# Optimization experiments

Hardware: AMD Instinct MI355X
Metric: run time of the kernel (lower is better)

## Reference

```python
import jax, jax.numpy as jnp
import numpy as np

RES = (512, 512)
MAX_VAL = 100.0
OBJ_WIDTH = 5
N_ITERS = 5
SIGMA = 0.2


def setup_inputs() -> dict:
    key = jax.random.key(0)
    ks = jax.random.split(key, 6)
    H, W = RES
    x = jax.random.uniform(ks[0], (1, H, W, 2), jnp.float32) * 2.0 - 1.0  # query grid in [-1,1]
    boundary_types = jax.random.randint(ks[1], (H, W), 0, 2, jnp.int32)
    boundary_conditions = jax.random.uniform(ks[2], (H, W), jnp.float32)
    B_enc = SIGMA * jax.random.normal(ks[3], (64, 2), jnp.float32)  # GaussianEncoding(0.2, 2, 64)
    Wh = jax.random.normal(ks[4], (4, 128, 128), jnp.float32) / jnp.sqrt(128.0)
    W_out = jax.random.normal(ks[5], (128, 1), jnp.float32) / jnp.sqrt(128.0)
    return {"x": x, "boundary_types": boundary_types,
            "boundary_conditions": boundary_conditions,
            "B_enc": B_enc, "Wh": Wh, "W_out": W_out}


def _box_filter(a, width):
    # width x width mean filter, 'same' padding (F.conv2d with ones/width^2 kernel)
    k = jnp.ones((1, 1, width, width), a.dtype) / float(width * width)
    return jax.lax.conv_general_dilated(a[None, None], k, (1, 1), "SAME")[0, 0]


def _grid_sample_2d(img, grid):
    # img [H,W]; grid [N,2] with (x,y) in [-1,1]; bilinear, align_corners=True, border padding
    H, W = img.shape
    ix = jnp.clip((grid[:, 0] + 1.0) * 0.5 * (W - 1), 0.0, W - 1.0)
    iy = jnp.clip((grid[:, 1] + 1.0) * 0.5 * (H - 1), 0.0, H - 1.0)
    x0 = jnp.floor(ix).astype(jnp.int32)
    y0 = jnp.floor(iy).astype(jnp.int32)
    x1 = jnp.clip(x0 + 1, 0, W - 1)
    y1 = jnp.clip(y0 + 1, 0, H - 1)
    wx = ix - x0
    wy = iy - y0
    return (img[y0, x0] * (1 - wx) * (1 - wy) + img[y0, x1] * wx * (1 - wy)
            + img[y1, x0] * (1 - wx) * wy + img[y1, x1] * wx * wy)


def _solve(V0, C, boundary_types, boundary_conditions):
    # 5 Jacobi-style 8-neighbor stencil passes: free cells take the neighbor
    # average plus local cost; boundary cells are pinned to their conditions.
    free = boundary_types == 0

    def step(V, _):
        Vp = jnp.pad(V, 1, mode="edge")
        nb = (Vp[:-2, :-2] + Vp[:-2, 1:-1] + Vp[:-2, 2:]
              + Vp[1:-1, :-2] + Vp[1:-1, 2:]
              + Vp[2:, :-2] + Vp[2:, 1:-1] + Vp[2:, 2:]) / 8.0
        return jnp.where(free, nb + C, boundary_conditions), None

    V, _ = jax.lax.scan(step, V0, None, length=N_ITERS)
    return V


def reference(x, boundary_types, boundary_conditions, B_enc, Wh, W_out):
    H, W = RES
    free = boundary_types == 0
    # V init: max_val everywhere, boundary cells pinned (obj_inds = boundary_types > 0)
    V0 = jnp.where(free, jnp.float32(MAX_VAL), boundary_conditions)

    # Gaussian random Fourier feature encoding of 0.5 + 0.5*x -> 128 dims
    xq = 0.5 + 0.5 * x.reshape(-1, 2)
    vp = (2.0 * jnp.pi) * (xq @ B_enc.T)            # [N, 64]
    enc = jnp.concatenate([jnp.cos(vp), jnp.sin(vp)], axis=-1)  # [N, 128]

    # FullyFusedMLP: 4 hidden ReLU layers of 128 neurons, linear 1-dim output, no bias
    h = enc
    for i in range(Wh.shape[0]):
        h = jax.nn.relu(h @ Wh[i])
    C = (h @ W_out).reshape(H, W)
    C_pos = jax.nn.relu(C)

    # extra cost: box-filtered obstacle boundary values splashed onto free cells
    obj = boundary_conditions * (boundary_types == 1) * (boundary_conditions > 0)
    extra = _box_filter(obj, OBJ_WIDTH) * free
    Cs = C_pos + extra

    out_grid = _solve(V0, Cs, boundary_types, boundary_conditions)
    out = _grid_sample_2d(out_grid, x.reshape(-1, 2)).reshape(H, W)
    return out, C
```

## Files before the change

### kernel.cpp

```cpp
#include <hip/hip_runtime.h>
#include <hip/hip_bf16.h>


typedef unsigned short ushort_t;
typedef short short8 __attribute__((ext_vector_type(8)));
typedef float floatx4 __attribute__((ext_vector_type(4)));

#define HH 512
#define WW 512
#define NPIX (HH*WW)

#define SW(p, f) (((p) << 7) + (((((f) >> 3) ^ ((p) & 15))) << 3) + ((f) & 7))

__device__ inline unsigned int pk_bf16(float a, float b) {
    __hip_bfloat162 h = __float22bfloat162_rn(float2{a, b});
    return *(unsigned int*)&h;
}
__device__ inline float bf2f(ushort_t u) {
    union { unsigned int i; float f; } v; v.i = ((unsigned int)u) << 16; return v.f;
}
__device__ inline void async_copy16(void* lds, const void* g) {
    __builtin_amdgcn_global_load_lds(
        (const __attribute__((address_space(1))) unsigned int*)g,
        (__attribute__((address_space(3))) unsigned int*)lds, 16, 0, 0);
}

__global__ __launch_bounds__(256) void prep_kernel(const float* __restrict__ Wh,
                                                   ushort_t* __restrict__ WT) {
    __shared__ float trans[64 * 33];
    const int tid = threadIdx.x;
    const int l = blockIdx.x >> 3, ng = (blockIdx.x >> 2) & 1, kq = blockIdx.x & 3;
    const int n0 = ng * 64, k0 = kq * 32;
    const int ln = tid & 63, wv = tid >> 6;
    #pragma unroll
    for (int pass = 0; pass < 8; ++pass) {
        int k = k0 + pass * 4 + wv;
        trans[ln * 33 + (k - k0)] = Wh[l * 16384 + k * 128 + n0 + ln];
    }
    __syncthreads();
    {
        int nl = tid >> 2, q = tid & 3;
        int n = n0 + nl;
        int lc = kq * 4 + q;
        int pc = lc ^ (n & 15);
        unsigned int w[4];
        #pragma unroll
        for (int j = 0; j < 4; ++j)
            w[j] = pk_bf16(trans[nl * 33 + q * 8 + 2 * j], trans[nl * 33 + q * 8 + 2 * j + 1]);
        *(uint4*)&WT[(l * 128 + n) * 128 + pc * 8] = uint4{w[0], w[1], w[2], w[3]};
    }
}

__global__ __launch_bounds__(256, 2) void mlp_kernel(const float* __restrict__ x,
                                                     const ushort_t* __restrict__ WT,
                                                     const float* __restrict__ benc,
                                                     const float* __restrict__ wout,
                                                     float* __restrict__ C_ws,
                                                     float* __restrict__ outbuf) {
    __shared__ __align__(16) ushort_t act[128 * 128];
    __shared__ __align__(16) ushort_t wbuf[128 * 128];
    const int tid = threadIdx.x;
    const int p0 = blockIdx.x * 128;
    const int lane = tid & 63, wave = tid >> 6;

    {
        const char* src = (const char*)WT;
        int base = wave * 512;
        #pragma unroll
        for (int c2 = 0; c2 < 8; ++c2) {
            int cb = base + c2 * 64;
            async_copy16(&wbuf[cb * 8], src + (cb + lane) * 16);
        }
    }

    {
        int p = tid & 127, h = tid >> 7;
        float2 xv = ((const float2*)x)[p0 + p];
        float xq0 = 0.5f + 0.5f * xv.x, xq1 = 0.5f + 0.5f * xv.y;
        const float4* b4 = (const float4*)benc;
        #pragma unroll 4
        for (int f2 = 0; f2 < 32; f2 += 2) {
            int f = h * 32 + f2;
            float4 b = b4[f >> 1];
            float t0 = __builtin_amdgcn_fractf(xq0 * b.x + xq1 * b.y);
            float t1 = __builtin_amdgcn_fractf(xq0 * b.z + xq1 * b.w);
            float s0 = __builtin_amdgcn_sinf(t0), c0 = __builtin_amdgcn_cosf(t0);
            float s1 = __builtin_amdgcn_sinf(t1), c1 = __builtin_amdgcn_cosf(t1);
            *(unsigned int*)&act[SW(p, f)]      = pk_bf16(c0, c1);
            *(unsigned int*)&act[SW(p, f + 64)] = pk_bf16(s0, s1);
        }
    }

    const int quad = lane >> 4, l16 = lane & 15;
    const int ntb = (wave >> 1) * 64;
    const int ptb = (wave & 1) * 64;

    #pragma unroll 1
    for (int l = 0; l < 4; ++l) {
        __syncthreads();

        floatx4 acc[4][4];
        #pragma unroll
        for (int i = 0; i < 4; ++i)
            #pragma unroll
            for (int j = 0; j < 4; ++j)
                acc[i][j] = floatx4{0.0f, 0.0f, 0.0f, 0.0f};

        #pragma unroll
        for (int ks = 0; ks < 4; ++ks) {
            int cs = ks * 4 + quad;
            short8 af[4], bv[4];
            #pragma unroll
            for (int i = 0; i < 4; ++i) {
                int r = ntb + i * 16 + l16;
                af[i] = *(const short8*)&wbuf[(r << 7) + ((cs ^ l16) << 3)];
            }
            #pragma unroll
            for (int j = 0; j < 4; ++j) {
                int p = ptb + j * 16 + l16;
                bv[j] = *(const short8*)&act[(p << 7) + ((cs ^ l16) << 3)];
            }
            #pragma unroll
            for (int i = 0; i < 4; ++i)
                #pragma unroll
                for (int j = 0; j < 4; ++j)
                    acc[i][j] = __builtin_amdgcn_mfma_f32_16x16x32_bf16(af[i], bv[j], acc[i][j], 0, 0, 0);
        }
        __syncthreads();

        if (l < 3) {
            const char* src = (const char*)WT + (l + 1) * 32768;
            int base = wave * 512;
            #pragma unroll
            for (int c2 = 0; c2 < 8; ++c2) {
                int cb = base + c2 * 64;
                async_copy16(&wbuf[cb * 8], src + (cb + lane) * 16);
            }
        }

        #pragma unroll
        for (int i = 0; i < 4; ++i) {
            #pragma unroll
            for (int j = 0; j < 4; ++j) {
                int p = ptb + j * 16 + l16;
                int n0 = ntb + i * 16 + quad * 4;
                uint2 pk;
                pk.x = pk_bf16(fmaxf(acc[i][j][0], 0.0f), fmaxf(acc[i][j][1], 0.0f));
                pk.y = pk_bf16(fmaxf(acc[i][j][2], 0.0f), fmaxf(acc[i][j][3], 0.0f));
                *(uint2*)&act[SW(p, n0)] = pk;
            }
        }
    }
    __syncthreads();

    {
        int p = tid >> 1, h = tid & 1;
        const float4* wo4 = (const float4*)wout;
        float sum = 0.0f;
        #pragma unroll
        for (int g = 0; g < 8; ++g) {
            int ch = h * 8 + g;
            short8 v = *(const short8*)&act[(p << 7) + ((ch ^ (p & 15)) << 3)];
            float4 wa = wo4[ch * 2], wb = wo4[ch * 2 + 1];
            sum += bf2f((ushort_t)v[0]) * wa.x + bf2f((ushort_t)v[1]) * wa.y
                 + bf2f((ushort_t)v[2]) * wa.z + bf2f((ushort_t)v[3]) * wa.w
                 + bf2f((ushort_t)v[4]) * wb.x + bf2f((ushort_t)v[5]) * wb.y
                 + bf2f((ushort_t)v[6]) * wb.z + bf2f((ushort_t)v[7]) * wb.w;
        }
        float other = __shfl_xor(sum, 1);
        if (h == 0) {
            float tot = sum + other;
            C_ws[p0 + p] = tot;
            outbuf[NPIX + p0 + p] = tot;
        }
    }
}

__global__ __launch_bounds__(256) void fused_solve_kernel(const int* __restrict__ bt,
                                                          const float* __restrict__ bc,
                                                          const float* __restrict__ C_ws,
                                                          float* __restrict__ Vfin) {
    __shared__ float Va[30 * 32];
    __shared__ float Vb[30 * 32];
    __shared__ float Wp[30 * 32];
    const int tid = threadIdx.x;
    const int gx0 = (blockIdx.x & 31) * 16 - 7, gy0 = (blockIdx.x >> 5) * 16 - 7;

    for (int c = tid; c < 30 * 32; c += 256) {
        int li = c >> 5, lj = c & 31;
        int gi = gy0 + li, gj = gx0 + lj;
        float v = 0.0f;
        if (lj < 30 && gi >= 0 && gi < HH && gj >= 0 && gj < WW) {
            int g = gi * WW + gj;
            float b = bc[g];
            if (bt[g] == 1 && b > 0.0f) v = b;
        }
        Va[c] = v;
    }
    __syncthreads();

    for (int c = tid; c < 30 * 32; c += 256) {
        int li = c >> 5, lj = c & 31;
        int gi = gy0 + li, gj = gx0 + lj;
        float w = -1.0f, v0 = 0.0f;
        if (li >= 2 && li < 28 && lj >= 2 && lj < 28 &&
            gi >= 0 && gi < HH && gj >= 0 && gj < WW) {
            int g = gi * WW + gj;
            if (bt[g] == 0) {
                float s = 0.0f;
                #pragma unroll
                for (int di = 0; di < 5; ++di)
                    #pragma unroll
                    for (int dj = 0; dj < 5; ++dj)
                        s += Va[(li + di - 2) * 32 + lj + dj - 2];
                w = fmaxf(C_ws[g], 0.0f) + s * 0.04f;
                v0 = 100.0f;
            } else {
                float b = bc[g];
                w = -b - 1.0f;
                v0 = b;
            }
        }
        Wp[c] = w;
        Vb[c] = v0;
    }
    __syncthreads();

    float* src = Vb;
    float* dst = Va;
    #pragma unroll 1
    for (int t = 0; t < 5; ++t) {
        for (int c = tid; c < 26 * 32; c += 256) {
            int li = 2 + (c >> 5), lj = c & 31;
            if (lj < 2 || lj >= 28) continue;
            float w = Wp[li * 32 + lj];
            float v;
            if (w < 0.0f) {
                v = -w - 1.0f;
            } else {
                int gi = gy0 + li, gj = gx0 + lj;
                int um = (gi > 0)      ? li - 1 : li;
                int dp = (gi < HH - 1) ? li + 1 : li;
                int lm = (gj > 0)      ? lj - 1 : lj;
                int rp = (gj < WW - 1) ? lj + 1 : lj;
                float s = src[um * 32 + lm] + src[um * 32 + lj] + src[um * 32 + rp]
                        + src[li * 32 + lm]                     + src[li * 32 + rp]
                        + src[dp * 32 + lm] + src[dp * 32 + lj] + src[dp * 32 + rp];
                v = s * 0.125f + w;
            }
            dst[li * 32 + lj] = v;
        }
        __syncthreads();
        float* tmp = src; src = dst; dst = tmp;
    }

    {
        int li = 7 + (tid >> 4), lj = 7 + (tid & 15);
        Vfin[(gy0 + li) * WW + gx0 + lj] = src[li * 32 + lj];
    }
}

__global__ void sample_kernel(const float* __restrict__ x,
                              const float* __restrict__ V,
                              float* __restrict__ out) {
    int idx = blockIdx.x * 256 + threadIdx.x;
    float2 g2 = ((const float2*)x)[idx];
    float ix = (g2.x + 1.0f) * 0.5f * 511.0f;
    float iy = (g2.y + 1.0f) * 0.5f * 511.0f;
    ix = fminf(fmaxf(ix, 0.0f), 511.0f);
    iy = fminf(fmaxf(iy, 0.0f), 511.0f);
    int x0 = (int)floorf(ix), y0 = (int)floorf(iy);
    int x1 = min(x0 + 1, 511), y1 = min(y0 + 1, 511);
    float wx = ix - (float)x0, wy = iy - (float)y0;
    float v00 = V[y0 * 512 + x0], v01 = V[y0 * 512 + x1];
    float v10 = V[y1 * 512 + x0], v11 = V[y1 * 512 + x1];
    float v = v00 * (1.0f - wx) * (1.0f - wy) + v01 * wx * (1.0f - wy)
            + v10 * (1.0f - wx) * wy          + v11 * wx * wy;
    out[idx] = v;
}

extern "C" void kernel_launch(void* const* d_in, const int* in_sizes, int n_in,
                              void* d_out, int out_size, void* d_ws, size_t ws_size,
                              hipStream_t stream) {
    const float* x    = (const float*)d_in[0];
    const int*   bt   = (const int*)d_in[1];
    const float* bc   = (const float*)d_in[2];
    const float* benc = (const float*)d_in[3];
    const float* Wh   = (const float*)d_in[4];
    const float* wout = (const float*)d_in[5];

    char* ws = (char*)d_ws;
    ushort_t* WT   = (ushort_t*)(ws + 4096);
    float*    C_ws = (float*)(ws + 262144);
    float*    Vfin = (float*)(ws + 262144 + 3 * (1 << 20));
    float*    outp = (float*)d_out;

    prep_kernel<<<32, 256, 0, stream>>>(Wh, WT);
    mlp_kernel<<<2048, 256, 0, stream>>>(x, WT, benc, wout, C_ws, outp);
    fused_solve_kernel<<<1024, 256, 0, stream>>>(bt, bc, C_ws, Vfin);
    sample_kernel<<<1024, 256, 0, stream>>>(x, Vfin, outp);
}
```

Baseline: 130.4 us.

## Halve MLP pixel tile and fuse output projection into register epilogue

Each MLP block now handles 64 pixels instead of 128, which halves the activation LDS buffer and raises launch bounds to three blocks per CU across twice as many blocks. The final 128-to-1 projection is computed straight from the last layer's fp32 MFMA accumulators with cross-lane shuffles and a small LDS reduction. This skips the bf16 write-back and re-read of the last activation and keeps that layer in fp32. The cost is that each block reloads the full weight matrices for half as many pixels, doubling weight traffic per pixel and giving less MFMA work per weight load.

Result: no change. 128.5 us (-1.4%).

```diff
diff --git a/kernel.cpp b/kernel.cpp
--- a/kernel.cpp
+++ b/kernel.cpp
@@ -51,16 +51,17 @@
     }
 }
 
-__global__ __launch_bounds__(256, 2) void mlp_kernel(const float* __restrict__ x,
+__global__ __launch_bounds__(256, 3) void mlp_kernel(const float* __restrict__ x,
                                                      const ushort_t* __restrict__ WT,
                                                      const float* __restrict__ benc,
                                                      const float* __restrict__ wout,
                                                      float* __restrict__ C_ws,
                                                      float* __restrict__ outbuf) {
-    __shared__ __align__(16) ushort_t act[128 * 128];
+    __shared__ __align__(16) ushort_t act[64 * 128];
     __shared__ __align__(16) ushort_t wbuf[128 * 128];
+    __shared__ float pbuf[4 * 32];
     const int tid = threadIdx.x;
-    const int p0 = blockIdx.x * 128;
+    const int p0 = blockIdx.x * 64;
     const int lane = tid & 63, wave = tid >> 6;
 
     {
@@ -74,13 +75,13 @@
     }
 
     {
-        int p = tid & 127, h = tid >> 7;
+        int p = tid & 63, h = tid >> 6;
         float2 xv = ((const float2*)x)[p0 + p];
         float xq0 = 0.5f + 0.5f * xv.x, xq1 = 0.5f + 0.5f * xv.y;
         const float4* b4 = (const float4*)benc;
         #pragma unroll 4
-        for (int f2 = 0; f2 < 32; f2 += 2) {
-            int f = h * 32 + f2;
+        for (int f2 = 0; f2 < 16; f2 += 2) {
+            int f = h * 16 + f2;
             float4 b = b4[f >> 1];
             float t0 = __builtin_amdgcn_fractf(xq0 * b.x + xq1 * b.y);
             float t1 = __builtin_amdgcn_fractf(xq0 * b.z + xq1 * b.w);
@@ -93,42 +94,44 @@
 
     const int quad = lane >> 4, l16 = lane & 15;
     const int ntb = (wave >> 1) * 64;
-    const int ptb = (wave & 1) * 64;
-
+    const int ptb = (wave & 1) * 32;
+
+    floatx4 acc[4][2];
     #pragma unroll 1
     for (int l = 0; l < 4; ++l) {
         __syncthreads();
 
-        floatx4 acc[4][4];
         #pragma unroll
         for (int i = 0; i < 4; ++i)
             #pragma unroll
-            for (int j = 0; j < 4; ++j)
+            for (int j = 0; j < 2; ++j)
                 acc[i][j] = floatx4{0.0f, 0.0f, 0.0f, 0.0f};
 
         #pragma unroll
         for (int ks = 0; ks < 4; ++ks) {
             int cs = ks * 4 + quad;
-            short8 af[4], bv[4];
+            short8 af[4], bv[2];
             #pragma unroll
             for (int i = 0; i < 4; ++i) {
                 int r = ntb + i * 16 + l16;
                 af[i] = *(const short8*)&wbuf[(r << 7) + ((cs ^ l16) << 3)];
             }
             #pragma unroll
-            for (int j = 0; j < 4; ++j) {
+            for (int j = 0; j < 2; ++j) {
                 int p = ptb + j * 16 + l16;
                 bv[j] = *(const short8*)&act[(p << 7) + ((cs ^ l16) << 3)];
             }
             #pragma unroll
             for (int i = 0; i < 4; ++i)
                 #pragma unroll
-                for (int j = 0; j < 4; ++j)
+                for (int j = 0; j < 2; ++j)
                     acc[i][j] = __builtin_amdgcn_mfma_f32_16x16x32_bf16(af[i], bv[j], acc[i][j], 0, 0, 0);
         }
+
+        if (l == 3) break;
         __syncthreads();
 
-        if (l < 3) {
+        {
             const char* src = (const char*)WT + (l + 1) * 32768;
             int base = wave * 512;
             #pragma unroll
@@ -141,7 +144,7 @@
         #pragma unroll
         for (int i = 0; i < 4; ++i) {
             #pragma unroll
-            for (int j = 0; j < 4; ++j) {
+            for (int j = 0; j < 2; ++j) {
                 int p = ptb + j * 16 + l16;
                 int n0 = ntb + i * 16 + quad * 4;
                 uint2 pk;
@@ -151,28 +154,34 @@
             }
         }
     }
+
+    {
+        float4 wv[4];
+        #pragma unroll
+        for (int i = 0; i < 4; ++i)
+            wv[i] = *(const float4*)&wout[ntb + i * 16 + quad * 4];
+        #pragma unroll
+        for (int j = 0; j < 2; ++j) {
+            float s = 0.0f;
+            #pragma unroll
+            for (int i = 0; i < 4; ++i) {
+                s += fmaxf(acc[i][j][0], 0.0f) * wv[i].x
+                   + fmaxf(acc[i][j][1], 0.0f) * wv[i].y
+                   + fmaxf(acc[i][j][2], 0.0f) * wv[i].z
+                   + fmaxf(acc[i][j][3], 0.0f) * wv[i].w;
+            }
+            s += __shfl_xor(s, 16);
+            s += __shfl_xor(s, 32);
+            if (quad == j) pbuf[wave * 32 + j * 16 + l16] = s;
+        }
+    }
     __syncthreads();
-
-    {
-        int p = tid >> 1, h = tid & 1;
-        const float4* wo4 = (const float4*)wout;
-        float sum = 0.0f;
-        #pragma unroll
-        for (int g = 0; g < 8; ++g) {
-            int ch = h * 8 + g;
-            short8 v = *(const short8*)&act[(p << 7) + ((ch ^ (p & 15)) << 3)];
-            float4 wa = wo4[ch * 2], wb = wo4[ch * 2 + 1];
-            sum += bf2f((ushort_t)v[0]) * wa.x + bf2f((ushort_t)v[1]) * wa.y
-                 + bf2f((ushort_t)v[2]) * wa.z + bf2f((ushort_t)v[3]) * wa.w
-                 + bf2f((ushort_t)v[4]) * wb.x + bf2f((ushort_t)v[5]) * wb.y
-                 + bf2f((ushort_t)v[6]) * wb.z + bf2f((ushort_t)v[7]) * wb.w;
-        }
-        float other = __shfl_xor(sum, 1);
-        if (h == 0) {
-            float tot = sum + other;
-            C_ws[p0 + p] = tot;
-            outbuf[NPIX + p0 + p] = tot;
-        }
+    if (tid < 64) {
+        int p = tid;
+        int half = p >> 5, idx = p & 31;
+        float tot = pbuf[half * 32 + idx] + pbuf[(half + 2) * 32 + idx];
+        C_ws[p0 + p] = tot;
+        outbuf[NPIX + p0 + p] = tot;
     }
 }
 
@@ -296,7 +305,7 @@
     float*    outp = (float*)d_out;
 
     prep_kernel<<<32, 256, 0, stream>>>(Wh, WT);
-    mlp_kernel<<<2048, 256, 0, stream>>>(x, WT, benc, wout, C_ws, outp);
+    mlp_kernel<<<4096, 256, 0, stream>>>(x, WT, benc, wout, C_ws, outp);
     fused_solve_kernel<<<1024, 256, 0, stream>>>(bt, bc, C_ws, Vfin);
     sample_kernel<<<1024, 256, 0, stream>>>(x, Vfin, outp);
 }
```
